# Performance work log

Measured on AMD Instinct MI355X. Metric: run time of the kernel, lower is better.

Reference implementation:

```python
import jax, jax.numpy as jnp
import numpy as np

B, C, H, W = 4, 64, 64, 64

def setup_inputs() -> dict:
    key = jax.random.key(0)
    ks = jax.random.split(key, 7)
    s = 1.0 / np.sqrt(C)
    return {
        "x": jax.random.normal(ks[0], (B, C, H, W), dtype=jnp.float32),
        "Wq": jax.random.normal(ks[1], (C, C), dtype=jnp.float32) * s,
        "bq": jax.random.normal(ks[2], (C,), dtype=jnp.float32) * s,
        "Wk": jax.random.normal(ks[3], (C, C), dtype=jnp.float32) * s,
        "bk": jax.random.normal(ks[4], (C,), dtype=jnp.float32) * s,
        "Wv": jax.random.normal(ks[5], (C, C), dtype=jnp.float32) * s,
        "bv": jax.random.normal(ks[6], (C,), dtype=jnp.float32) * s,
    }

def reference(x, Wq, bq, Wk, bk, Wv, bv):
    b, c, h, w = x.shape
    n = h * w
    xf = x.reshape(b, c, n)                                   # (B,C,N)
    # 1x1 convs == per-pixel linear maps over channels
    q = jnp.einsum('oc,bcn->bon', Wq, xf) + bq[None, :, None]  # (B,C,N)
    k = jnp.einsum('oc,bcn->bon', Wk, xf) + bk[None, :, None]  # (B,C,N)
    v = jnp.einsum('oc,bcn->bon', Wv, xf) + bv[None, :, None]  # (B,C,N)
    # energy = Q^T K : (B,N,N); note: no 1/sqrt(C) scaling in the original
    energy = jnp.einsum('bcn,bcm->bnm', q, k)
    attention = jax.nn.softmax(energy, axis=-1)
    # out = V @ attention^T : out[:, :, i] = sum_j V[:, :, j] * attention[i, j]
    out = jnp.einsum('bcm,bnm->bcn', v, attention)
    return out.reshape(b, c, h, w)
```

## Files before the change

### kernel.cpp

```cpp
#include <hip/hip_runtime.h>
#include <math.h>

#define T_N 4096
#define T_C 64
#define T_B 4
#define NSLICE 8
#define TILES_PER_SLICE (64 / NSLICE)

typedef __attribute__((ext_vector_type(8))) _Float16 f16x8;
typedef __attribute__((ext_vector_type(4))) _Float16 f16x4;
typedef __attribute__((ext_vector_type(4))) float f32x4;

__device__ inline unsigned short f2h(float f) {
    union { _Float16 h; unsigned short s; } u; u.h = (_Float16)f; return u.s;
}
__device__ inline float h2f(unsigned short s) {
    union { unsigned short s; _Float16 h; } u; u.s = s; return (float)u.h;
}

__global__ __launch_bounds__(256) void qkv_kernel(
    const float* __restrict__ x,
    const float* __restrict__ Wq, const float* __restrict__ bq,
    const float* __restrict__ Wk, const float* __restrict__ bk,
    const float* __restrict__ Wv, const float* __restrict__ bv,
    unsigned short* __restrict__ qt, unsigned short* __restrict__ kt,
    unsigned short* __restrict__ vb)
{
    __shared__ __align__(16) unsigned short xsh[32 * 72];
    __shared__ __align__(16) unsigned short xsl[32 * 72];
    __shared__ __align__(16) unsigned short wf[3][64 * 72];

    const int tid = threadIdx.x;
    const int n0  = blockIdx.x * 32;
    const int b   = blockIdx.y;
    const float* xb = x + (size_t)b * T_C * T_N;

    const float* Ws[3] = {Wq, Wk, Wv};
    #pragma unroll
    for (int p = 0; p < 3; ++p) {
        for (int i = tid; i < 1024; i += 256) {
            const int o = i >> 4, c4 = (i & 15) * 4;
            const float4 w4 = ((const float4*)Ws[p])[i];
            f16x4 wh;
            wh[0] = (_Float16)w4.x; wh[1] = (_Float16)w4.y;
            wh[2] = (_Float16)w4.z; wh[3] = (_Float16)w4.w;
            *(f16x4*)&wf[p][o * 72 + c4] = wh;
        }
    }
    for (int i = tid; i < 512; i += 256) {
        const int c = i >> 3, nj4 = (i & 7) * 4;
        const float4 xv = *(const float4*)&xb[c * T_N + n0 + nj4];
        const float xa[4] = {xv.x, xv.y, xv.z, xv.w};
        #pragma unroll
        for (int j = 0; j < 4; ++j) {
            const unsigned short h = f2h(xa[j]);
            xsh[(nj4 + j) * 72 + c] = h;
            xsl[(nj4 + j) * 72 + c] = f2h(xa[j] - h2f(h));
        }
    }
    __syncthreads();

    const int wv_  = tid >> 6;
    const int lane = tid & 63;
    const int quad = lane >> 4;
    const int col  = lane & 15;
    const int pst  = (wv_ & 1) * 16;
    const int oh   = (wv_ >> 1) * 2;
    const size_t bN = (size_t)b * T_N;

    f16x8 xh[2], xl[2];
    #pragma unroll
    for (int s = 0; s < 2; ++s) {
        xh[s] = *(const f16x8*)&xsh[(pst + col) * 72 + s * 32 + quad * 8];
        xl[s] = *(const f16x8*)&xsl[(pst + col) * 72 + s * 32 + quad * 8];
    }
    __syncthreads();

    const float* biases[3] = {bq, bk, bv};
    for (int p = 0; p < 3; ++p) {
        #pragma unroll
        for (int oo = 0; oo < 2; ++oo) {
            const int osub = oh + oo;
            f32x4 acc = (f32x4){0.f, 0.f, 0.f, 0.f};
            #pragma unroll
            for (int s = 0; s < 2; ++s) {
                const f16x8 wfr =
                    *(const f16x8*)&wf[p][(osub * 16 + col) * 72 + s * 32 + quad * 8];
                acc = __builtin_amdgcn_mfma_f32_16x16x32_f16(xh[s], wfr, acc, 0, 0, 0);
                acc = __builtin_amdgcn_mfma_f32_16x16x32_f16(xl[s], wfr, acc, 0, 0, 0);
            }
            const float bb = biases[p][osub * 16 + col];
            if (p < 2) {
                #pragma unroll
                for (int r = 0; r < 4; ++r)
                    xsh[(pst + quad * 4 + r) * 72 + osub * 16 + col] = f2h(acc[r] + bb);
            } else {
                union { ushort4 v; unsigned short s[4]; } hv;
                #pragma unroll
                for (int r = 0; r < 4; ++r) hv.s[r] = f2h(acc[r] + bb);
                *(ushort4*)&xsh[(osub * 16 + col) * 36 + pst + quad * 4] = hv.v;
            }
        }
        __syncthreads();
        if (p < 2) {
            const int pix = tid >> 3, c8 = (tid & 7) * 8;
            unsigned short* dst = (p == 0) ? qt : kt;
            *(f16x8*)&dst[(bN + n0 + pix) * 64 + c8] = *(const f16x8*)&xsh[pix * 72 + c8];
            __syncthreads();
        } else {
            const int o = tid >> 2, p8 = (tid & 3) * 8;
            *(f16x8*)&vb[((size_t)(b * 64 + o)) * T_N + n0 + p8] =
                *(const f16x8*)&xsh[o * 36 + p8];
        }
    }
}

__global__ __launch_bounds__(256, 4) void attn_kernel(
    const unsigned short* __restrict__ qt,
    const unsigned short* __restrict__ kt, const unsigned short* __restrict__ vb,
    unsigned short* __restrict__ o_part, float* __restrict__ mp, float* __restrict__ lp)
{
    __shared__ __align__(16) unsigned short ks[64 * 64];
    __shared__ __align__(16) unsigned short vs[64 * 64];

    const int tid   = threadIdx.x;
    const int n0    = blockIdx.x * 128;
    const int slice = blockIdx.y;
    const int b     = blockIdx.z;
    const int wv_   = tid >> 6;
    const int lane  = tid & 63;
    const int quad  = lane >> 4;
    const int col   = lane & 15;

    const size_t bN = (size_t)b * T_N;
    const int q0 = n0 + wv_ * 32 + col;
    const int q1 = q0 + 16;

    f16x8 qh0[2], qh1[2];
    #pragma unroll
    for (int s = 0; s < 2; ++s) {
        qh0[s] = *(const f16x8*)&qt[(bN + q0) * 64 + s * 32 + quad * 8];
        qh1[s] = *(const f16x8*)&qt[(bN + q1) * 64 + s * 32 + quad * 8];
    }

    const int row = tid >> 3, cc = tid & 7;
    const int pc  = (cc ^ (row & 7)) * 8;

    const int mbase = slice * TILES_PER_SLICE * 64;
    float4 p0, p1, p2, p3;
    p0 = *(const float4*)&kt[(bN + mbase + row) * 64 + cc * 8];
    p1 = *(const float4*)&kt[(bN + mbase + 32 + row) * 64 + cc * 8];
    p2 = *(const float4*)&vb[((size_t)(b * 64 + row)) * T_N + mbase + cc * 8];
    p3 = *(const float4*)&vb[((size_t)(b * 64 + 32 + row)) * T_N + mbase + cc * 8];

    f32x4 O0[4], O1[4];
    #pragma unroll
    for (int t = 0; t < 4; ++t) {
        O0[t] = (f32x4){0.f, 0.f, 0.f, 0.f};
        O1[t] = (f32x4){0.f, 0.f, 0.f, 0.f};
    }
    float m_st0 = -INFINITY, l_st0 = 0.f;
    float m_st1 = -INFINITY, l_st1 = 0.f;

    for (int it = 0; it < TILES_PER_SLICE; ++it) {
        __syncthreads();
        *(float4*)&ks[row * 64 + pc]        = p0;
        *(float4*)&ks[(32 + row) * 64 + pc] = p1;
        *(float4*)&vs[row * 64 + pc]        = p2;
        *(float4*)&vs[(32 + row) * 64 + pc] = p3;
        __syncthreads();

        {
            const int itn = (it + 1 < TILES_PER_SLICE) ? it + 1 : it;
            const int m0n = mbase + itn * 64;
            p0 = *(const float4*)&kt[(bN + m0n + row) * 64 + cc * 8];
            p1 = *(const float4*)&kt[(bN + m0n + 32 + row) * 64 + cc * 8];
            p2 = *(const float4*)&vb[((size_t)(b * 64 + row)) * T_N + m0n + cc * 8];
            p3 = *(const float4*)&vb[((size_t)(b * 64 + 32 + row)) * T_N + m0n + cc * 8];
        }

        f32x4 acc0[4], acc1[4];
        #pragma unroll
        for (int t = 0; t < 4; ++t) {
            acc0[t] = (f32x4){0.f, 0.f, 0.f, 0.f};
            acc1[t] = (f32x4){0.f, 0.f, 0.f, 0.f};
        }
        #pragma unroll
        for (int s = 0; s < 2; ++s) {
            #pragma unroll
            for (int t = 0; t < 4; ++t) {
                const f16x8 kf = *(const f16x8*)
                    &ks[(t * 16 + col) * 64 + (((s * 4 + quad) ^ (col & 7)) * 8)];
                acc0[t] = __builtin_amdgcn_mfma_f32_16x16x32_f16(kf, qh0[s], acc0[t], 0, 0, 0);
                acc1[t] = __builtin_amdgcn_mfma_f32_16x16x32_f16(kf, qh1[s], acc1[t], 0, 0, 0);
            }
        }

        f16x4 pf0[4], pf1[4];
        float alpha0, alpha1;
        {
            float mx = -INFINITY;
            #pragma unroll
            for (int t = 0; t < 4; ++t)
                #pragma unroll
                for (int r = 0; r < 4; ++r) mx = fmaxf(mx, acc0[t][r]);
            mx = fmaxf(mx, __shfl_xor(mx, 16));
            mx = fmaxf(mx, __shfl_xor(mx, 32));
            const float mnew = fmaxf(m_st0, mx);
            alpha0 = __expf(m_st0 - mnew);
            float sum = 0.f;
            #pragma unroll
            for (int t = 0; t < 4; ++t) {
                #pragma unroll
                for (int r = 0; r < 4; ++r) {
                    const float pv = __expf(acc0[t][r] - mnew);
                    sum += pv;
                    pf0[t][r] = (_Float16)pv;
                }
            }
            sum += __shfl_xor(sum, 16);
            sum += __shfl_xor(sum, 32);
            l_st0 = alpha0 * l_st0 + sum;
            m_st0 = mnew;
        }
        {
            float mx = -INFINITY;
            #pragma unroll
            for (int t = 0; t < 4; ++t)
                #pragma unroll
                for (int r = 0; r < 4; ++r) mx = fmaxf(mx, acc1[t][r]);
            mx = fmaxf(mx, __shfl_xor(mx, 16));
            mx = fmaxf(mx, __shfl_xor(mx, 32));
            const float mnew = fmaxf(m_st1, mx);
            alpha1 = __expf(m_st1 - mnew);
            float sum = 0.f;
            #pragma unroll
            for (int t = 0; t < 4; ++t) {
                #pragma unroll
                for (int r = 0; r < 4; ++r) {
                    const float pv = __expf(acc1[t][r] - mnew);
                    sum += pv;
                    pf1[t][r] = (_Float16)pv;
                }
            }
            sum += __shfl_xor(sum, 16);
            sum += __shfl_xor(sum, 32);
            l_st1 = alpha1 * l_st1 + sum;
            m_st1 = mnew;
        }

        #pragma unroll
        for (int tc = 0; tc < 4; ++tc) {
            O0[tc] *= alpha0;
            O1[tc] *= alpha1;
            #pragma unroll
            for (int t = 0; t < 4; ++t) {
                const f16x4 vf = *(const f16x4*)
                    &vs[(tc * 16 + col) * 64 +
                        (((2 * t + (quad >> 1)) ^ (col & 7)) * 8) + (quad & 1) * 4];
                O0[tc] = __builtin_amdgcn_mfma_f32_16x16x16f16(vf, pf0[t], O0[tc], 0, 0, 0);
                O1[tc] = __builtin_amdgcn_mfma_f32_16x16x16f16(vf, pf1[t], O1[tc], 0, 0, 0);
            }
        }
    }

    const size_t srow = (size_t)(slice * T_B + b) * 64;
    #pragma unroll
    for (int tc = 0; tc < 4; ++tc) {
        #pragma unroll
        for (int r = 0; r < 4; ++r) {
            const size_t crow = (srow + tc * 16 + quad * 4 + r) * T_N;
            o_part[crow + q0] = f2h(O0[tc][r]);
            o_part[crow + q1] = f2h(O1[tc][r]);
        }
    }
    if (quad == 0) {
        const size_t off = (size_t)(slice * T_B + b) * T_N;
        mp[off + q0] = m_st0;
        lp[off + q0] = l_st0;
        mp[off + q1] = m_st1;
        lp[off + q1] = l_st1;
    }
}

__global__ __launch_bounds__(256) void combine_kernel(
    const unsigned short* __restrict__ o_part,
    const float* __restrict__ mp, const float* __restrict__ lp,
    float* __restrict__ out)
{
    __shared__ float wn[NSLICE][32];

    const int tid = threadIdx.x;
    const int n0  = blockIdx.x * 32;
    const int b   = blockIdx.y;

    if (tid < 32) {
        float m_s[NSLICE], l_s[NSLICE];
        #pragma unroll
        for (int s = 0; s < NSLICE; ++s) {
            const size_t off = (size_t)(s * T_B + b) * T_N + n0 + tid;
            m_s[s] = mp[off];
            l_s[s] = lp[off];
        }
        float M = m_s[0];
        #pragma unroll
        for (int s = 1; s < NSLICE; ++s) M = fmaxf(M, m_s[s]);
        float w_s[NSLICE], L = 0.f;
        #pragma unroll
        for (int s = 0; s < NSLICE; ++s) {
            w_s[s] = __expf(m_s[s] - M);
            L += l_s[s] * w_s[s];
        }
        const float inv = 1.f / L;
        #pragma unroll
        for (int s = 0; s < NSLICE; ++s) wn[s][tid] = w_s[s] * inv;
    }
    __syncthreads();

    for (int t = tid; t < 512; t += 256) {
        const int c = t >> 3, g = t & 7;
        float4 acc = make_float4(0.f, 0.f, 0.f, 0.f);
        #pragma unroll
        for (int s = 0; s < NSLICE; ++s) {
            const ushort4 o4 = *(const ushort4*)
                &o_part[((size_t)((s * T_B + b) * 64 + c)) * T_N + n0 + g * 4];
            acc.x = fmaf(h2f(o4.x), wn[s][g * 4 + 0], acc.x);
            acc.y = fmaf(h2f(o4.y), wn[s][g * 4 + 1], acc.y);
            acc.z = fmaf(h2f(o4.z), wn[s][g * 4 + 2], acc.z);
            acc.w = fmaf(h2f(o4.w), wn[s][g * 4 + 3], acc.w);
        }
        *(float4*)&out[((size_t)(b * 64 + c)) * T_N + n0 + g * 4] = acc;
    }
}

extern "C" void kernel_launch(void* const* d_in, const int* in_sizes, int n_in,
                              void* d_out, int out_size, void* d_ws, size_t ws_size,
                              hipStream_t stream) {
    const float* x  = (const float*)d_in[0];
    const float* Wq = (const float*)d_in[1];
    const float* bq = (const float*)d_in[2];
    const float* Wk = (const float*)d_in[3];
    const float* bk = (const float*)d_in[4];
    const float* Wv = (const float*)d_in[5];
    const float* bv = (const float*)d_in[6];
    float* outp = (float*)d_out;

    const size_t elems = (size_t)T_B * T_N * T_C;
    unsigned short* qtp    = (unsigned short*)d_ws;
    unsigned short* ktp    = qtp + elems;
    unsigned short* vbuf   = ktp + elems;
    unsigned short* o_part = vbuf + elems;
    float* mp = (float*)(o_part + (size_t)NSLICE * elems);
    float* lp = mp + (size_t)NSLICE * T_B * T_N;

    qkv_kernel<<<dim3(T_N / 32, T_B), 256, 0, stream>>>(
        x, Wq, bq, Wk, bk, Wv, bv, qtp, ktp, vbuf);
    attn_kernel<<<dim3(T_N / 128, NSLICE, T_B), 256, 0, stream>>>(
        qtp, ktp, vbuf, o_part, mp, lp);
    combine_kernel<<<dim3(T_N / 32, T_B), 256, 0, stream>>>(
        o_part, mp, lp, outp);
}
```

Baseline: 112.0 us.

## Fuse split-K combine into attention kernel via last-block atomic counter

Measured after the change: 268.8 us. 2.4x slower.

```diff
diff --git a/kernel.cpp b/kernel.cpp
--- a/kernel.cpp
+++ b/kernel.cpp
@@ -6,6 +6,7 @@
 #define T_B 4
 #define NSLICE 8
 #define TILES_PER_SLICE (64 / NSLICE)
+#define NQGRP (T_N / 128)
 
 typedef __attribute__((ext_vector_type(8))) _Float16 f16x8;
 typedef __attribute__((ext_vector_type(4))) _Float16 f16x4;
@@ -118,10 +119,13 @@
 __global__ __launch_bounds__(256, 4) void attn_kernel(
     const unsigned short* __restrict__ qt,
     const unsigned short* __restrict__ kt, const unsigned short* __restrict__ vb,
-    unsigned short* __restrict__ o_part, float* __restrict__ mp, float* __restrict__ lp)
+    unsigned short* __restrict__ o_part, float* __restrict__ mp,
+    float* __restrict__ lp, unsigned int* __restrict__ cnt,
+    float* __restrict__ out)
 {
     __shared__ __align__(16) unsigned short ks[64 * 64];
     __shared__ __align__(16) unsigned short vs[64 * 64];
+    __shared__ unsigned int is_last;
 
     const int tid   = threadIdx.x;
     const int n0    = blockIdx.x * 128;
@@ -281,20 +285,18 @@
         mp[off + q1] = m_st1;
         lp[off + q1] = l_st1;
     }
-}
-
-__global__ __launch_bounds__(256) void combine_kernel(
-    const unsigned short* __restrict__ o_part,
-    const float* __restrict__ mp, const float* __restrict__ lp,
-    float* __restrict__ out)
-{
-    __shared__ float wn[NSLICE][32];
-
-    const int tid = threadIdx.x;
-    const int n0  = blockIdx.x * 32;
-    const int b   = blockIdx.y;
-
-    if (tid < 32) {
+
+    __threadfence();
+    if (tid == 0) {
+        const unsigned old = atomicAdd(&cnt[b * NQGRP + blockIdx.x], 1u);
+        is_last = (old == NSLICE - 1) ? 1u : 0u;
+    }
+    __syncthreads();
+    if (!is_last) return;
+    __threadfence();
+
+    float* wn = (float*)ks;
+    if (tid < 128) {
         float m_s[NSLICE], l_s[NSLICE];
         #pragma unroll
         for (int s = 0; s < NSLICE; ++s) {
@@ -313,23 +315,23 @@
         }
         const float inv = 1.f / L;
         #pragma unroll
-        for (int s = 0; s < NSLICE; ++s) wn[s][tid] = w_s[s] * inv;
+        for (int s = 0; s < NSLICE; ++s) wn[s * 128 + tid] = w_s[s] * inv;
     }
     __syncthreads();
 
-    for (int t = tid; t < 512; t += 256) {
-        const int c = t >> 3, g = t & 7;
-        float4 acc = make_float4(0.f, 0.f, 0.f, 0.f);
+    for (int t2 = tid; t2 < 2048; t2 += 256) {
+        const int c = t2 >> 5, g = t2 & 31;
+        float4 acc2 = make_float4(0.f, 0.f, 0.f, 0.f);
         #pragma unroll
         for (int s = 0; s < NSLICE; ++s) {
             const ushort4 o4 = *(const ushort4*)
                 &o_part[((size_t)((s * T_B + b) * 64 + c)) * T_N + n0 + g * 4];
-            acc.x = fmaf(h2f(o4.x), wn[s][g * 4 + 0], acc.x);
-            acc.y = fmaf(h2f(o4.y), wn[s][g * 4 + 1], acc.y);
-            acc.z = fmaf(h2f(o4.z), wn[s][g * 4 + 2], acc.z);
-            acc.w = fmaf(h2f(o4.w), wn[s][g * 4 + 3], acc.w);
-        }
-        *(float4*)&out[((size_t)(b * 64 + c)) * T_N + n0 + g * 4] = acc;
+            acc2.x = fmaf(h2f(o4.x), wn[s * 128 + g * 4 + 0], acc2.x);
+            acc2.y = fmaf(h2f(o4.y), wn[s * 128 + g * 4 + 1], acc2.y);
+            acc2.z = fmaf(h2f(o4.z), wn[s * 128 + g * 4 + 2], acc2.z);
+            acc2.w = fmaf(h2f(o4.w), wn[s * 128 + g * 4 + 3], acc2.w);
+        }
+        *(float4*)&out[((size_t)(b * 64 + c)) * T_N + n0 + g * 4] = acc2;
     }
 }
 
@@ -345,18 +347,18 @@
     const float* bv = (const float*)d_in[6];
     float* outp = (float*)d_out;
 
+    unsigned int* cnt = (unsigned int*)d_ws;
     const size_t elems = (size_t)T_B * T_N * T_C;
-    unsigned short* qtp    = (unsigned short*)d_ws;
+    unsigned short* qtp    = (unsigned short*)((char*)d_ws + 1024);
     unsigned short* ktp    = qtp + elems;
     unsigned short* vbuf   = ktp + elems;
     unsigned short* o_part = vbuf + elems;
     float* mp = (float*)(o_part + (size_t)NSLICE * elems);
     float* lp = mp + (size_t)NSLICE * T_B * T_N;
 
+    hipMemsetAsync(cnt, 0, T_B * NQGRP * sizeof(unsigned int), stream);
     qkv_kernel<<<dim3(T_N / 32, T_B), 256, 0, stream>>>(
         x, Wq, bq, Wk, bk, Wv, bv, qtp, ktp, vbuf);
     attn_kernel<<<dim3(T_N / 128, NSLICE, T_B), 256, 0, stream>>>(
-        qtp, ktp, vbuf, o_part, mp, lp);
-    combine_kernel<<<dim3(T_N / 32, T_B), 256, 0, stream>>>(
-        o_part, mp, lp, outp);
-}
+        qtp, ktp, vbuf, o_part, mp, lp, cnt, outp);
+}
```
